# Optimization experiments

Hardware: AMD Instinct MI355X
Metric: run time of the kernel (lower is better)

## Reference

```python
import jax, jax.numpy as jnp
import numpy as np

GROUPS = 32
EPS = 1e-5


def setup_inputs() -> dict:
    key = jax.random.key(0)
    ks = jax.random.split(key, 7)
    B, C, H, W = 32, 512, 32, 32
    x = jax.random.normal(ks[0], (B, C, H, W), dtype=jnp.float32)
    # GroupNorm affine params
    gn_w = jnp.ones((C,), dtype=jnp.float32)
    gn_b = jnp.zeros((C,), dtype=jnp.float32)
    # 1x1 Conv1d == matmul over channel dim
    qkv_w = jax.random.normal(ks[1], (3 * C, C), dtype=jnp.float32) * (C ** -0.5)
    qkv_b = jax.random.normal(ks[2], (3 * C,), dtype=jnp.float32) * 0.02
    proj_w = jax.random.normal(ks[3], (C, C), dtype=jnp.float32) * (C ** -0.5)
    proj_b = jax.random.normal(ks[4], (C,), dtype=jnp.float32) * 0.02
    return {"x": x, "gn_w": gn_w, "gn_b": gn_b, "qkv_w": qkv_w,
            "qkv_b": qkv_b, "proj_w": proj_w, "proj_b": proj_b}


def _group_norm(x, w, b):
    B, C, H, W = x.shape
    xg = x.reshape(B, GROUPS, C // GROUPS, H, W)
    mean = xg.mean(axis=(2, 3, 4), keepdims=True)
    var = xg.var(axis=(2, 3, 4), keepdims=True)
    xg = (xg - mean) * jax.lax.rsqrt(var + EPS)
    return xg.reshape(B, C, H, W) * w[None, :, None, None] + b[None, :, None, None]


def reference(x, gn_w, gn_b, qkv_w, qkv_b, proj_w, proj_b):
    B, C, H, W = x.shape
    h = _group_norm(x, gn_w, gn_b).reshape(B, C, H * W)  # [B, C, N]
    qkv = jnp.einsum('oc,bcn->bon', qkv_w, h) + qkv_b[None, :, None]  # [B, 3C, N]
    q, k, v = jnp.split(qkv, 3, axis=1)
    scale = C ** (-0.5)
    # scores: q^T k  -> [B, N, N]
    attn = jax.nn.softmax(jnp.einsum('bcn,bcm->bnm', q, k) * scale, axis=-1)
    # h = v @ attn^T -> [B, C, N]
    h = jnp.einsum('bcm,bnm->bcn', v, attn)
    h = jnp.einsum('oc,bcn->bon', proj_w, h) + proj_b[None, :, None]
    return x + h.reshape(B, C, H, W)
```

## Files before the change

kernel.cpp:

```cpp
#include <hip/hip_runtime.h>
#include <stdint.h>

typedef __bf16 bf16;
typedef __bf16 bf16x4 __attribute__((ext_vector_type(4)));
typedef __bf16 bf16x8 __attribute__((ext_vector_type(8)));
typedef float f32x4 __attribute__((ext_vector_type(4)));

#define CN 524288
#define NPIX 1024
#define CCH 512

__device__ __forceinline__ void gload_lds16(const void* g, void* l) {
  auto gp = reinterpret_cast<const __attribute__((address_space(1))) uint32_t*>(
      reinterpret_cast<uintptr_t>(g));
  auto lp = reinterpret_cast<__attribute__((address_space(3))) uint32_t*>(
      static_cast<uint32_t>(reinterpret_cast<uintptr_t>(l)));
  __builtin_amdgcn_global_load_lds(gp, lp, 16, 0, 0);
}

template<int EPI>
__global__ __launch_bounds__(512, 2)
void gemm_bt(const bf16* __restrict__ A, int lda, long long sA,
             const bf16* __restrict__ Bt, int ldb, long long sB,
             char* __restrict__ Cp, long long sC,
             char* __restrict__ C2p, long long sC2,
             const float* __restrict__ bias,
             const float* __restrict__ resid,
             float* __restrict__ pst,
             int K, float scale)
{
  __shared__ __align__(16) bf16 As[2 * 16384];
  __shared__ __align__(16) bf16 Bs[2 * 16384];
  const int t = threadIdx.x;
  const int w = t >> 6;
  const int l = t & 63;

  const int gx = gridDim.x, gy = gridDim.y;
  const int nwg = gx * gy * gridDim.z;
  int lin = blockIdx.x + gx * (blockIdx.y + gy * blockIdx.z);
  lin = (lin & 7) * (nwg >> 3) + (lin >> 3);
  const int bx = lin % gx;
  const int by = (lin / gx) % gy;
  const int z  = lin / (gx * gy);

  A  += (long long)z * sA;
  Bt += (long long)z * sB;
  Cp += (long long)z * sC;
  if (C2p) C2p += (long long)z * sC2;
  const float* residb = (EPI == 3) ? (resid + (long long)z * CN) : nullptr;

  const int row0 = bx * 256;
  const int col0 = by * 256;
  const int wr = w >> 2;
  const int wc = w & 3;

  f32x4 acc[8][4] = {};

  const int wv  = w;
  const int srow = (l >> 3);
  const int segp = ((l & 7) ^ srow) << 3;
  const bf16* baseA = A  + (long long)(row0 + wv * 8 + srow) * lda + segp;
  const bf16* baseB = Bt + (long long)(col0 + wv * 8 + srow) * ldb + segp;

  auto stageA = [&](int kt1, int buf, int c) {
    gload_lds16(baseA + (long long)c * 64 * lda + kt1 * 64,
                &As[buf * 16384 + c * 4096 + wv * 512]);
  };
  auto stageB = [&](int kt1, int buf, int c) {
    gload_lds16(baseB + (long long)c * 64 * ldb + kt1 * 64,
                &Bs[buf * 16384 + c * 4096 + wv * 512]);
  };

  const int lrow = l & 15;
  const int lx = l & 7;
  const int s0 = (((l >> 4)) ^ lx) << 3;
  const int s1 = (((l >> 4) + 4) ^ lx) << 3;

  const int nt = K >> 6;

  #pragma unroll
  for (int c = 0; c < 4; ++c) stageB(0, 0, c);
  #pragma unroll
  for (int c = 0; c < 4; ++c) stageA(0, 0, c);

  #pragma unroll 1
  for (int kt = 0; kt < nt; ++kt) {
    const int cur = kt & 1, nxt = cur ^ 1;
    const bool pf = (kt + 1) < nt;
    if (pf) {
      #pragma unroll
      for (int c = 0; c < 4; ++c) stageB(kt + 1, nxt, c);
      asm volatile("s_waitcnt vmcnt(4)" ::: "memory");
    } else {
      asm volatile("s_waitcnt vmcnt(0)" ::: "memory");
    }
    __builtin_amdgcn_sched_barrier(0);
    __builtin_amdgcn_s_barrier();
    asm volatile("" ::: "memory");

    const int ca = cur * 16384;
    bf16x8 bF0[4], bF1[4], aF0[4], aF1[4];
    #pragma unroll
    for (int nf = 0; nf < 4; ++nf) {
      const int r = wc * 64 + nf * 16 + lrow;
      bF0[nf] = *(const bf16x8*)&Bs[ca + r * 64 + s0];
      bF1[nf] = *(const bf16x8*)&Bs[ca + r * 64 + s1];
    }
    #pragma unroll
    for (int mf = 0; mf < 4; ++mf) {
      const int r = wr * 128 + mf * 16 + lrow;
      aF0[mf] = *(const bf16x8*)&As[ca + r * 64 + s0];
      aF1[mf] = *(const bf16x8*)&As[ca + r * 64 + s1];
    }
    __builtin_amdgcn_s_setprio(1);
    #pragma unroll
    for (int mf = 0; mf < 4; ++mf)
      #pragma unroll
      for (int nf = 0; nf < 4; ++nf)
        acc[mf][nf] = __builtin_amdgcn_mfma_f32_16x16x32_bf16(
            aF1[mf], bF1[nf],
            __builtin_amdgcn_mfma_f32_16x16x32_bf16(aF0[mf], bF0[nf], acc[mf][nf], 0, 0, 0),
            0, 0, 0);
    __builtin_amdgcn_s_setprio(0);
    if (pf) {
      #pragma unroll
      for (int c = 0; c < 4; ++c) stageA(kt + 1, nxt, c);
    }
    #pragma unroll
    for (int mf = 0; mf < 4; ++mf) {
      const int r = wr * 128 + 64 + mf * 16 + lrow;
      aF0[mf] = *(const bf16x8*)&As[ca + r * 64 + s0];
      aF1[mf] = *(const bf16x8*)&As[ca + r * 64 + s1];
    }
    __builtin_amdgcn_s_setprio(1);
    #pragma unroll
    for (int mf = 0; mf < 4; ++mf)
      #pragma unroll
      for (int nf = 0; nf < 4; ++nf)
        acc[4 + mf][nf] = __builtin_amdgcn_mfma_f32_16x16x32_bf16(
            aF1[mf], bF1[nf],
            __builtin_amdgcn_mfma_f32_16x16x32_bf16(aF0[mf], bF0[nf], acc[4 + mf][nf], 0, 0, 0),
            0, 0, 0);
    __builtin_amdgcn_s_setprio(0);
    asm volatile("" ::: "memory");
    __builtin_amdgcn_sched_barrier(0);
    __builtin_amdgcn_s_barrier();
  }

  const int ci = (l >> 4) * 4;
  const int cj = l & 15;

  if constexpr (EPI == 1) {
    bf16* sp = (bf16*)Cp;
    float* part = (float*)As;
    #pragma unroll
    for (int mf = 0; mf < 8; ++mf) {
      const int lr0 = wr * 128 + mf * 16 + ci;
      #pragma unroll
      for (int r = 0; r < 4; ++r) {
        float s = 0.f;
        #pragma unroll
        for (int nf = 0; nf < 4; ++nf) {
          const int j = col0 + wc * 64 + nf * 16 + cj;
          const float u = __expf(acc[mf][nf][r] * scale);
          const bf16 ub = (bf16)u;
          sp[(row0 + lr0 + r) * NPIX + j] = ub;
          s += (float)ub;
        }
        s += __shfl_xor(s, 1); s += __shfl_xor(s, 2);
        s += __shfl_xor(s, 4); s += __shfl_xor(s, 8);
        if (cj == 0) part[wc * 256 + lr0 + r] = s;
      }
    }
    __syncthreads();
    if (t < 256)
      pst[((long long)z * 4 + by) * 1024 + row0 + t]
          = part[t] + part[256 + t] + part[512 + t] + part[768 + t];
    return;
  }

  #pragma unroll
  for (int mf = 0; mf < 8; ++mf) {
    const int i0 = row0 + wr * 128 + mf * 16 + ci;
    if constexpr (EPI == 2) {
      const float* pz = pst + (long long)z * 4096;
      #pragma unroll
      for (int r = 0; r < 4; ++r) {
        const int row = i0 + r;
        const float is = 1.f / (pz[row] + pz[1024 + row] +
                                pz[2048 + row] + pz[3072 + row]);
        bf16* hp = (bf16*)Cp;
        #pragma unroll
        for (int nf = 0; nf < 4; ++nf) {
          const int j = col0 + wc * 64 + nf * 16 + cj;
          hp[row * CCH + j] = (bf16)(acc[mf][nf][r] * is);
        }
      }
    } else {
      #pragma unroll
      for (int nf = 0; nf < 4; ++nf) {
        const int j = col0 + wc * 64 + nf * 16 + cj;
        const f32x4 a = acc[mf][nf];
        if constexpr (EPI == 0) {
          const float bj = bias[j];
          if (j < NPIX) {
            bf16* q = (bf16*)Cp;
            #pragma unroll
            for (int r = 0; r < 4; ++r)
              q[(i0 + r) * NPIX + j] = (bf16)(a[r] + bj);
          } else {
            bf16* vb = (bf16*)C2p;
            #pragma unroll
            for (int r = 0; r < 4; ++r)
              vb[(j - NPIX) * NPIX + (i0 + r)] = (bf16)(a[r] + bj);
          }
        } else {
          float* op = (float*)Cp;
          #pragma unroll
          for (int r = 0; r < 4; ++r)
            op[(i0 + r) * NPIX + j] = a[r] + bias[i0 + r] + residb[(i0 + r) * NPIX + j];
        }
      }
    }
  }
}

__global__ __launch_bounds__(512)
void gn_fused(const float* __restrict__ x, const float* __restrict__ gw,
              const float* __restrict__ gb, bf16* __restrict__ hnT)
{
  __shared__ float xs[16 * 1024];
  __shared__ float red[16];
  const int b = blockIdx.x >> 5;
  const int g = blockIdx.x & 31;
  const float* xp = x + ((long long)b * CCH + g * 16) * NPIX;
  const int t = threadIdx.x;

  float4* xsv = (float4*)xs;
  const float4* gv = (const float4*)xp;
  float s = 0.f, ss = 0.f;
  #pragma unroll
  for (int i = 0; i < 8; ++i) {
    float4 v = gv[t + i * 512];
    xsv[t + i * 512] = v;
    s  += v.x + v.y + v.z + v.w;
    ss += v.x * v.x + v.y * v.y + v.z * v.z + v.w * v.w;
  }
  #pragma unroll
  for (int o = 32; o; o >>= 1) { s += __shfl_xor(s, o); ss += __shfl_xor(ss, o); }
  if ((t & 63) == 0) { red[t >> 6] = s; red[8 + (t >> 6)] = ss; }
  __syncthreads();
  s  = red[0] + red[1] + red[2] + red[3] + red[4] + red[5] + red[6] + red[7];
  ss = red[8] + red[9] + red[10] + red[11] + red[12] + red[13] + red[14] + red[15];
  const float mean = s * (1.f / 16384.f);
  const float var  = ss * (1.f / 16384.f) - mean * mean;
  const float rstd = rsqrtf(var + 1e-5f);

  float ac[16], bc[16];
  #pragma unroll
  for (int c = 0; c < 16; ++c) {
    const float wv = gw[g * 16 + c] * rstd;
    ac[c] = wv;
    bc[c] = gb[g * 16 + c] - mean * wv;
  }

  bf16* hp = hnT + (long long)b * 1048576;
  hp += g * 16;
  #pragma unroll
  for (int r = 0; r < 2; ++r) {
    const int n = t + r * 512;
    bf16x8 o0, o1;
    #pragma unroll
    for (int c = 0; c < 8; ++c)
      o0[c] = (bf16)(xs[c * 1024 + n] * ac[c] + bc[c]);
    #pragma unroll
    for (int c = 0; c < 8; ++c)
      o1[c] = (bf16)(xs[(8 + c) * 1024 + n] * ac[8 + c] + bc[8 + c]);
    *(bf16x8*)&hp[(long long)n * CCH]     = o0;
    *(bf16x8*)&hp[(long long)n * CCH + 8] = o1;
  }
}

__global__ __launch_bounds__(256)
void cvt_weights(const float* __restrict__ qw, const float* __restrict__ pw,
                 bf16* __restrict__ qwb, bf16* __restrict__ pwb)
{
  const int i = blockIdx.x * 256 + threadIdx.x;
  if (i < 3 * CCH * CCH) qwb[i] = (bf16)qw[i];
  if (i < CCH * CCH) pwb[i] = (bf16)pw[i];
}

extern "C" void kernel_launch(void* const* d_in, const int* in_sizes, int n_in,
                              void* d_out, int out_size, void* d_ws, size_t ws_size,
                              hipStream_t stream)
{
  const float* x      = (const float*)d_in[0];
  const float* gn_w   = (const float*)d_in[1];
  const float* gn_b   = (const float*)d_in[2];
  const float* qkv_w  = (const float*)d_in[3];
  const float* qkv_b  = (const float*)d_in[4];
  const float* proj_w = (const float*)d_in[5];
  const float* proj_b = (const float*)d_in[6];
  float* out = (float*)d_out;
  (void)in_sizes; (void)n_in; (void)out_size;

  char* ws = (char*)d_ws;
  size_t off = 0;
  auto alloc = [&](size_t bytes) -> char* {
    char* p = ws + off;
    off += (bytes + 255) & ~(size_t)255;
    return p;
  };
  bf16* qkv_wb  = (bf16*)alloc(3 * 512 * 512 * 2);
  bf16* proj_wb = (bf16*)alloc(512 * 512 * 2);
  const size_t fixed = off;
  const size_t per = 2097152ull + 2097152ull + 1048576ull + 16384ull;
  int Bc = 32;
  if (ws_size > fixed) {
    size_t fit = (ws_size - fixed) / per;
    if (fit < 32) Bc = (int)fit;
  } else {
    Bc = 0;
  }
  if (Bc < 1) Bc = 1;

  char* regA = alloc((size_t)Bc * 2097152);
  char* regB = alloc((size_t)Bc * 2097152);
  bf16*  vbuf   = (bf16*) alloc((size_t)Bc * 1048576);
  float* pstats = (float*)alloc((size_t)Bc * 16384);
  bf16* hnT  = (bf16*)regA;
  bf16* ubuf = (bf16*)regA;
  bf16* qkT  = (bf16*)regB;
  bf16* hvT  = (bf16*)regB;

  cvt_weights<<<dim3(3072), 256, 0, stream>>>(qkv_w, proj_w, qkv_wb, proj_wb);

  const float scale = 0.044194173824159216f;
  for (int b0 = 0; b0 < 32; b0 += Bc) {
    const int bc = (32 - b0 < Bc) ? (32 - b0) : Bc;
    const float* xb = x + (size_t)b0 * CN;

    gn_fused<<<dim3(bc * 32), 512, 0, stream>>>(xb, gn_w, gn_b, hnT);

    gemm_bt<0><<<dim3(4, 6, bc), 512, 0, stream>>>(
        hnT, 512, 1048576, qkv_wb, 512, 0,
        (char*)qkT, 2097152, (char*)vbuf, 1048576, qkv_b, nullptr, nullptr,
        512, 1.f);

    gemm_bt<1><<<dim3(4, 4, bc), 512, 0, stream>>>(
        qkT, 1024, 1048576, qkT + 512, 1024, 1048576,
        (char*)ubuf, 2097152, nullptr, 0, nullptr, nullptr, pstats,
        512, scale);

    gemm_bt<2><<<dim3(4, 2, bc), 512, 0, stream>>>(
        ubuf, 1024, 1048576, vbuf, 1024, 524288,
        (char*)hvT, 2097152, nullptr, 0, nullptr, nullptr, pstats,
        1024, 1.f);

    gemm_bt<3><<<dim3(2, 4, bc), 512, 0, stream>>>(
        proj_wb, 512, 0, hvT, 512, 1048576,
        (char*)(out + (size_t)b0 * CN), 2097152, nullptr, 0, proj_b, xb,
        nullptr, 512, 1.f);
  }
}
```

Before: 232.7 us.

## Fold output projection into V weights and fuse residual into PV epilogue

Precomputes Wpv = proj_w·Wv and bpv = proj_w·bv on the device so the V projection directly produces projected values. The attention-times-V GEMM epilogue then applies the softmax normalization, adds the folded bias (which passes through because softmax rows sum to one) and the residual, and writes the fp32 output. This removes the separate projection GEMM launch and the hvT intermediate round trip. In exchange it adds a small weight-product kernel on every call and rounds the folded weights to bf16, which changes numerics slightly.

```diff
diff --git a/kernel.cpp b/kernel.cpp
--- a/kernel.cpp
+++ b/kernel.cpp
@@ -47,7 +47,7 @@
   Bt += (long long)z * sB;
   Cp += (long long)z * sC;
   if (C2p) C2p += (long long)z * sC2;
-  const float* residb = (EPI == 3) ? (resid + (long long)z * CN) : nullptr;
+  const float* residb = (EPI == 2) ? (resid + (long long)z * CN) : nullptr;
 
   const int row0 = bx * 256;
   const int col0 = by * 256;
@@ -179,47 +179,54 @@
     return;
   }
 
+  if constexpr (EPI == 2) {
+    const float* pz = pst + (long long)z * 4096;
+    float* op = (float*)Cp;
+    #pragma unroll
+    for (int mf = 0; mf < 8; ++mf) {
+      const int i0 = row0 + wr * 128 + mf * 16 + ci;
+      float is[4];
+      #pragma unroll
+      for (int r = 0; r < 4; ++r) {
+        const int row = i0 + r;
+        is[r] = 1.f / (pz[row] + pz[1024 + row] +
+                       pz[2048 + row] + pz[3072 + row]);
+      }
+      #pragma unroll
+      for (int nf = 0; nf < 4; ++nf) {
+        const int j = col0 + wc * 64 + nf * 16 + cj;
+        const float bj = bias[j];
+        const float4 xv = *(const float4*)&residb[(long long)j * NPIX + i0];
+        float4 ov;
+        ov.x = acc[mf][nf][0] * is[0] + bj + xv.x;
+        ov.y = acc[mf][nf][1] * is[1] + bj + xv.y;
+        ov.z = acc[mf][nf][2] * is[2] + bj + xv.z;
+        ov.w = acc[mf][nf][3] * is[3] + bj + xv.w;
+        *(float4*)&op[(long long)j * NPIX + i0] = ov;
+      }
+    }
+    return;
+  }
+
   #pragma unroll
   for (int mf = 0; mf < 8; ++mf) {
     const int i0 = row0 + wr * 128 + mf * 16 + ci;
-    if constexpr (EPI == 2) {
-      const float* pz = pst + (long long)z * 4096;
-      #pragma unroll
-      for (int r = 0; r < 4; ++r) {
-        const int row = i0 + r;
-        const float is = 1.f / (pz[row] + pz[1024 + row] +
-                                pz[2048 + row] + pz[3072 + row]);
-        bf16* hp = (bf16*)Cp;
+    #pragma unroll
+    for (int nf = 0; nf < 4; ++nf) {
+      const int j = col0 + wc * 64 + nf * 16 + cj;
+      const f32x4 a = acc[mf][nf];
+      if (j < NPIX) {
+        const float bj = bias[j];
+        bf16* q = (bf16*)Cp;
         #pragma unroll
-        for (int nf = 0; nf < 4; ++nf) {
-          const int j = col0 + wc * 64 + nf * 16 + cj;
-          hp[row * CCH + j] = (bf16)(acc[mf][nf][r] * is);
-        }
-      }
-    } else {
-      #pragma unroll
-      for (int nf = 0; nf < 4; ++nf) {
-        const int j = col0 + wc * 64 + nf * 16 + cj;
-        const f32x4 a = acc[mf][nf];
-        if constexpr (EPI == 0) {
-          const float bj = bias[j];
-          if (j < NPIX) {
-            bf16* q = (bf16*)Cp;
-            #pragma unroll
-            for (int r = 0; r < 4; ++r)
-              q[(i0 + r) * NPIX + j] = (bf16)(a[r] + bj);
-          } else {
-            bf16* vb = (bf16*)C2p;
-            #pragma unroll
-            for (int r = 0; r < 4; ++r)
-              vb[(j - NPIX) * NPIX + (i0 + r)] = (bf16)(a[r] + bj);
-          }
-        } else {
-          float* op = (float*)Cp;
-          #pragma unroll
-          for (int r = 0; r < 4; ++r)
-            op[(i0 + r) * NPIX + j] = a[r] + bias[i0 + r] + residb[(i0 + r) * NPIX + j];
-        }
+        for (int r = 0; r < 4; ++r)
+          q[(i0 + r) * NPIX + j] = (bf16)(a[r] + bj);
+      } else {
+        const float bj = resid[j - NPIX];
+        bf16* vb = (bf16*)C2p;
+        #pragma unroll
+        for (int r = 0; r < 4; ++r)
+          vb[(j - NPIX) * NPIX + (i0 + r)] = (bf16)(a[r] + bj);
       }
     }
   }
@@ -282,12 +289,50 @@
 }
 
 __global__ __launch_bounds__(256)
-void cvt_weights(const float* __restrict__ qw, const float* __restrict__ pw,
-                 bf16* __restrict__ qwb, bf16* __restrict__ pwb)
+void prep_pv(const float* __restrict__ qkv_w, const float* __restrict__ qkv_b,
+             const float* __restrict__ proj_w,
+             bf16* __restrict__ wpv, float* __restrict__ bpv)
+{
+  const int c0 = blockIdx.x * 32;
+  const int d0 = blockIdx.y * 32;
+  const int t = threadIdx.x;
+  const float* Wv = qkv_w + 1024 * 512;
+  const int cc = c0 + (t >> 3);
+  const int d4 = d0 + (t & 7) * 4;
+
+  float a0 = 0.f, a1 = 0.f, a2 = 0.f, a3 = 0.f;
+  #pragma unroll 4
+  for (int o = 0; o < 512; ++o) {
+    const float p = proj_w[cc * 512 + o];
+    const float4 v4 = *(const float4*)&Wv[o * 512 + d4];
+    a0 += p * v4.x; a1 += p * v4.y; a2 += p * v4.z; a3 += p * v4.w;
+  }
+  bf16x4 w4;
+  w4[0] = (bf16)a0; w4[1] = (bf16)a1; w4[2] = (bf16)a2; w4[3] = (bf16)a3;
+  *(bf16x4*)&wpv[(long long)cc * 512 + d4] = w4;
+
+  if (blockIdx.y == 0) {
+    __shared__ float red[8][32];
+    const int og = t >> 5, ci2 = t & 31;
+    float s = 0.f;
+    for (int o = og * 64; o < og * 64 + 64; ++o)
+      s += proj_w[(c0 + ci2) * 512 + o] * qkv_b[1024 + o];
+    red[og][ci2] = s;
+    __syncthreads();
+    if (t < 32) {
+      float us = 0.f;
+      #pragma unroll
+      for (int i = 0; i < 8; ++i) us += red[i][t];
+      bpv[c0 + t] = us;
+    }
+  }
+}
+
+__global__ __launch_bounds__(256)
+void cvt_weights(const float* __restrict__ qw, bf16* __restrict__ qwb)
 {
   const int i = blockIdx.x * 256 + threadIdx.x;
-  if (i < 3 * CCH * CCH) qwb[i] = (bf16)qw[i];
-  if (i < CCH * CCH) pwb[i] = (bf16)pw[i];
+  if (i < 1024 * 512) qwb[i] = (bf16)qw[i];
 }
 
 extern "C" void kernel_launch(void* const* d_in, const int* in_sizes, int n_in,
@@ -311,8 +356,8 @@
     off += (bytes + 255) & ~(size_t)255;
     return p;
   };
-  bf16* qkv_wb  = (bf16*)alloc(3 * 512 * 512 * 2);
-  bf16* proj_wb = (bf16*)alloc(512 * 512 * 2);
+  bf16*  qkv_wb = (bf16*)alloc(1536 * 512 * 2);
+  float* bpv    = (float*)alloc(512 * 4);
   const size_t fixed = off;
   const size_t per = 2097152ull + 2097152ull + 1048576ull + 16384ull;
   int Bc = 32;
@@ -325,15 +370,15 @@
   if (Bc < 1) Bc = 1;
 
   char* regA = alloc((size_t)Bc * 2097152);
-  char* regB = alloc((size_t)Bc * 2097152);
+  bf16*  qkT    = (bf16*) alloc((size_t)Bc * 2097152);
   bf16*  vbuf   = (bf16*) alloc((size_t)Bc * 1048576);
   float* pstats = (float*)alloc((size_t)Bc * 16384);
   bf16* hnT  = (bf16*)regA;
   bf16* ubuf = (bf16*)regA;
-  bf16* qkT  = (bf16*)regB;
-  bf16* hvT  = (bf16*)regB;
-
-  cvt_weights<<<dim3(3072), 256, 0, stream>>>(qkv_w, proj_w, qkv_wb, proj_wb);
+
+  cvt_weights<<<dim3(2048), 256, 0, stream>>>(qkv_w, qkv_wb);
+  prep_pv<<<dim3(16, 16), 256, 0, stream>>>(qkv_w, qkv_b, proj_w,
+                                            qkv_wb + 1024 * 512, bpv);
 
   const float scale = 0.044194173824159216f;
   for (int b0 = 0; b0 < 32; b0 += Bc) {
@@ -344,7 +389,7 @@
 
     gemm_bt<0><<<dim3(4, 6, bc), 512, 0, stream>>>(
         hnT, 512, 1048576, qkv_wb, 512, 0,
-        (char*)qkT, 2097152, (char*)vbuf, 1048576, qkv_b, nullptr, nullptr,
+        (char*)qkT, 2097152, (char*)vbuf, 1048576, qkv_b, bpv, nullptr,
         512, 1.f);
 
     gemm_bt<1><<<dim3(4, 4, bc), 512, 0, stream>>>(
@@ -354,12 +399,7 @@
 
     gemm_bt<2><<<dim3(4, 2, bc), 512, 0, stream>>>(
         ubuf, 1024, 1048576, vbuf, 1024, 524288,
-        (char*)hvT, 2097152, nullptr, 0, nullptr, nullptr, pstats,
-        1024, 1.f);
-
-    gemm_bt<3><<<dim3(2, 4, bc), 512, 0, stream>>>(
-        proj_wb, 512, 0, hvT, 512, 1048576,
         (char*)(out + (size_t)b0 * CN), 2097152, nullptr, 0, proj_b, xb,
-        nullptr, 512, 1.f);
-  }
-}
+        pstats, 1024, 1.f);
+  }
+}
```

Result: slower. 281.5 us (+21.0%).
